# Optimization experiments

Hardware: AMD Instinct MI355X
Metric: run time of the kernel (lower is better)

Reference implementation:

```python
import jax, jax.numpy as jnp
import numpy as np

N_HEADS = 16
HEAD_DIM = 64
SEQ_LEN = 2048
BATCH = 1


def alibi_slopes(n_heads):
    start = 2.0 ** (-8.0 / n_heads)
    return jnp.asarray([start * start ** i for i in range(n_heads)], dtype=jnp.float32)


def setup_inputs() -> dict:
    key = jax.random.key(0)
    kq, kk, kv = jax.random.split(key, 3)
    shape = (BATCH, N_HEADS, SEQ_LEN, HEAD_DIM)
    return {
        "q": jax.random.normal(kq, shape, dtype=jnp.float32),
        "k": jax.random.normal(kk, shape, dtype=jnp.float32),
        "v": jax.random.normal(kv, shape, dtype=jnp.float32),
    }


def reference(q, k, v):
    # q,k,v: [B,H,S,D]
    seq_len = q.shape[2]
    head_dim = q.shape[3]
    scale = 1.0 / np.sqrt(head_dim).astype(np.float32)
    # scores: [B,H,S,S]
    scores = jnp.einsum("bhsd,bhtd->bhst", q, k) * scale
    pos = jnp.arange(seq_len)
    # distances[i, j] = j - i  (pos.unsqueeze(0) - pos.unsqueeze(1))
    distances = (pos[None, :] - pos[:, None]).astype(jnp.float32)  # [S,S]
    slopes = alibi_slopes(q.shape[1])  # [H]
    alibi = slopes[:, None, None] * distances[None, :, :]  # [H,S,S]
    scores = scores + alibi[None]
    attn = jax.nn.softmax(scores, axis=-1)
    return jnp.einsum("bhst,bhtd->bhsd", attn, v)
```

## Files before the change

### kernel.cpp

```cpp
#include <hip/hip_runtime.h>
#include <hip/hip_bf16.h>
#include <stdint.h>

#define N_HEADS 16
#define HEAD_DIM 64
#define SEQ_LEN 2048
#define KVBLK 64
#define NT 16
#define NTILE_TOT (SEQ_LEN / 32)

typedef __bf16 bf16x8 __attribute__((ext_vector_type(8)));
typedef __bf16 bf16x4 __attribute__((ext_vector_type(4)));
typedef short  s16x4  __attribute__((ext_vector_type(4)));
typedef float  f32x4  __attribute__((ext_vector_type(4)));
typedef unsigned int u32x4 __attribute__((ext_vector_type(4)));

#if __has_builtin(__builtin_amdgcn_mfma_f32_16x16x16bf16_1k)
#define HAVE_MFMA16 1
#else
#define HAVE_MFMA16 0
#endif

#if __has_builtin(__builtin_amdgcn_global_load_lds)
#define HAVE_GLL 1
#define GLL16(gsrc, ldst)                                                     \
    __builtin_amdgcn_global_load_lds(                                         \
        (const __attribute__((address_space(1))) void*)(gsrc),                \
        (__attribute__((address_space(3))) void*)(ldst), 16, 0, 0)
#else
#define HAVE_GLL 0
#endif

static __device__ __forceinline__ unsigned pkbf(float a, float b) {
    union { __bf16 h[2]; unsigned u; } t;
    t.h[0] = (__bf16)a; t.h[1] = (__bf16)b;
    return t.u;
}

static __device__ __forceinline__ int vpos(int k) {
#if HAVE_MFMA16
    return ((k & 12) << 2) + ((k & 16) >> 1) + ((k & 3) << 1);
#else
    return k * 2;
#endif
}

__global__ __launch_bounds__(256)
void prep_kernel(const float* __restrict__ k,
                 const float* __restrict__ v,
                 char* __restrict__ kimg,
                 char* __restrict__ vtimg) {
    const int ts  = blockIdx.x;
    const int h   = blockIdx.y;
    const int tid = threadIdx.x;
    const int s0  = ts * 32;
    const size_t blk = ((size_t)h * NTILE_TOT + ts) * 4096;

    const int krow = tid >> 3;
    const int kcol = (tid & 7) * 8;
    const float* ks = k + ((size_t)h * SEQ_LEN + s0 + krow) * HEAD_DIM + kcol;
    f32x4 a = *(const f32x4*)ks;
    f32x4 b = *(const f32x4*)(ks + 4);
    bf16x8 kb;
    #pragma unroll
    for (int i = 0; i < 4; ++i) { kb[i] = (__bf16)a[i]; kb[4 + i] = (__bf16)b[i]; }
    *(bf16x8*)(kimg + blk + krow * 128 + ((kcol * 2) ^ ((krow & 7) << 4))) = kb;

    const int vc = tid & 63;
    const int vr = (tid >> 6) * 8;
    const float* vs = v + ((size_t)h * SEQ_LEN + s0 + vr) * HEAD_DIM + vc;
    bf16x4 vb0, vb1;
    #pragma unroll
    for (int j = 0; j < 4; ++j) {
        vb0[j] = (__bf16)vs[(size_t)j * HEAD_DIM];
        vb1[j] = (__bf16)vs[(size_t)(4 + j) * HEAD_DIM];
    }
    const int swzV = (vc & 7) << 4;
    *(bf16x4*)(vtimg + blk + ((vc * 64 + vpos(vr))     ^ swzV)) = vb0;
    *(bf16x4*)(vtimg + blk + ((vc * 64 + vpos(vr + 4)) ^ swzV)) = vb1;
}

template <bool IMG>
__global__ __launch_bounds__(512, 2)
void attn_alibi_kernel(const float* __restrict__ q,
                       const float* __restrict__ k,
                       const float* __restrict__ v,
                       float* __restrict__ out,
                       const char* __restrict__ kimg,
                       const char* __restrict__ vtimg) {
    const int tid  = threadIdx.x;
    const int wave = tid >> 6;
    const int lane = tid & 63;
    const int col  = lane & 15;
    const int g    = lane >> 4;
    const int half = wave >> 2;
    const int w4   = wave & 3;

    const int h      = blockIdx.y;
    const int qbase  = blockIdx.x * 64 + w4 * 16;
    const int kstart = half * (NT * KVBLK);

    const float* qh = q + (size_t)h * SEQ_LEN * HEAD_DIM;
    const float* kh = k + (size_t)h * SEQ_LEN * HEAD_DIM;
    const float* vh = v + (size_t)h * SEQ_LEN * HEAD_DIM;

    __shared__ alignas(16) char smem[65536];
    char* kbase  = smem + half * 16384;
    char* vtbase = smem + 32768 + half * 16384;

    const float LOG2E  = 1.4426950408889634f;
    const float scale2 = 0.125f * LOG2E;
    const float slope  = exp2f(-0.5f * (float)(h + 1));
    const float slope2 = slope * LOG2E;

    bf16x8 qf[2];
    {
        const float* qr = qh + (size_t)(qbase + col) * HEAD_DIM + g * 8;
        #pragma unroll
        for (int c = 0; c < 2; ++c)
            #pragma unroll
            for (int b = 0; b < 8; ++b) qf[c][b] = (__bf16)qr[c * 32 + b];
    }

    float cb[4][4];
    #pragma unroll
    for (int i = 0; i < 4; ++i)
        #pragma unroll
        for (int r = 0; r < 4; ++r)
            cb[i][r] = slope2 * (float)(i * 16 + g * 4 + r - (qbase + col));

    float m = -1e30f, l = 0.0f;
    f32x4 acc[4];
    #pragma unroll
    for (int dt = 0; dt < 4; ++dt) acc[dt] = (f32x4)0.0f;

    const int hid  = tid & 255;
    const int krow = hid >> 3;
    const int kcol = (hid & 7) * 8;
    const int vc   = hid & 63;
    const int vr   = (hid >> 6) * 8;

    const char* kis = nullptr; const char* vis = nullptr;
    const float* ksrc = nullptr; const float* vsrc = nullptr;
    char* kdst = nullptr; char* vtdst0 = nullptr; char* vtdst1 = nullptr;
    if constexpr (IMG) {
        const size_t base = ((size_t)h * NTILE_TOT + half * (NTILE_TOT / 2)) * 4096
                          + hid * 16;
        kis = kimg + base;  vis = vtimg + base;
#if HAVE_GLL
        kdst   = kbase + w4 * 1024;
        vtdst0 = vtbase + w4 * 1024;
#else
        kdst   = kbase + hid * 16;
        vtdst0 = vtbase + hid * 16;
#endif
    } else {
        ksrc  = kh + (size_t)(kstart + krow) * HEAD_DIM + kcol;
        kdst  = kbase + krow * 128 + ((kcol * 2) ^ ((krow & 7) << 4));
        vsrc  = vh + (size_t)(kstart + vr) * HEAD_DIM + vc;
        const int swzV = (vc & 7) << 4;
        vtdst0 = vtbase + ((vc * 64 + vpos(vr))     ^ swzV);
        vtdst1 = vtbase + ((vc * 64 + vpos(vr + 4)) ^ swzV);
    }

    f32x4 kreg[2], vreg[2];
    f32x4 kr[2][2];
    float vv[2][8];

    if constexpr (IMG) {
#if HAVE_GLL
        #pragma unroll
        for (int sb = 0; sb < 2; ++sb) {
            GLL16(kis + sb * 4096, kdst   + sb * 4096);
            GLL16(vis + sb * 4096, vtdst0 + sb * 4096);
        }
#else
        #pragma unroll
        for (int sb = 0; sb < 2; ++sb) {
            kreg[sb] = *(const f32x4*)(kis + sb * 4096);
            vreg[sb] = *(const f32x4*)(vis + sb * 4096);
            *(f32x4*)(kdst   + sb * 4096) = kreg[sb];
            *(f32x4*)(vtdst0 + sb * 4096) = vreg[sb];
        }
#endif
    } else {
        #pragma unroll
        for (int sb = 0; sb < 2; ++sb) {
            const float* ks = ksrc + (size_t)(sb * 32) * HEAD_DIM;
            const float* vs = vsrc + (size_t)(sb * 32) * HEAD_DIM;
            kr[sb][0] = *(const f32x4*)(ks);
            kr[sb][1] = *(const f32x4*)(ks + 4);
            #pragma unroll
            for (int j = 0; j < 8; ++j) vv[sb][j] = vs[(size_t)j * HEAD_DIM];
            bf16x8 kb16;
            bf16x4 vb0, vb1;
            #pragma unroll
            for (int b = 0; b < 4; ++b) {
                kb16[b] = (__bf16)kr[sb][0][b]; kb16[4 + b] = (__bf16)kr[sb][1][b];
                vb0[b] = (__bf16)vv[sb][b];     vb1[b] = (__bf16)vv[sb][4 + b];
            }
            *(bf16x8*)(kdst   + sb * 4096) = kb16;
            *(bf16x4*)(vtdst0 + sb * 4096) = vb0;
            *(bf16x4*)(vtdst1 + sb * 4096) = vb1;
        }
    }
    __syncthreads();

    for (int t = 0; t < NT; ++t) {
        const int kb  = kstart + t * KVBLK;
        const int buf = t & 1;
        const char* kbuf  = kbase + buf * 8192;
        const char* vtbuf = vtbase + buf * 8192;

#if HAVE_GLL
        if (IMG && t + 1 < NT) {
            const int nb = (t + 1) & 1;
            #pragma unroll
            for (int sb = 0; sb < 2; ++sb) {
                GLL16(kis + (size_t)((t + 1) * 2 + sb) * 4096,
                      kdst + nb * 8192 + sb * 4096);
                GLL16(vis + (size_t)((t + 1) * 2 + sb) * 4096,
                      vtdst0 + nb * 8192 + sb * 4096);
            }
        }
#endif

        f32x4 sacc[4];
        #pragma unroll
        for (int i = 0; i < 4; ++i) sacc[i] = (f32x4)0.0f;
        __builtin_amdgcn_s_setprio(1);
        #pragma unroll
        for (int sb = 0; sb < 2; ++sb) {
            #pragma unroll
            for (int jt = 0; jt < 2; ++jt) {
                const int row = jt * 16 + col;
                const int i   = sb * 2 + jt;
                #pragma unroll
                for (int c = 0; c < 2; ++c) {
                    bf16x8 kf = *(const bf16x8*)(kbuf + sb * 4096 + row * 128
                                                 + ((c * 64 + g * 16) ^ ((row & 7) << 4)));
                    sacc[i] = __builtin_amdgcn_mfma_f32_16x16x32_bf16(kf, qf[c], sacc[i], 0, 0, 0);
                }
            }
        }
        __builtin_amdgcn_s_setprio(0);

        if (t + 1 < NT) {
            if constexpr (IMG) {
#if !HAVE_GLL
                #pragma unroll
                for (int sb = 0; sb < 2; ++sb) {
                    kreg[sb] = *(const f32x4*)(kis + (size_t)((t + 1) * 2 + sb) * 4096);
                    vreg[sb] = *(const f32x4*)(vis + (size_t)((t + 1) * 2 + sb) * 4096);
                }
#endif
            } else {
                #pragma unroll
                for (int sb = 0; sb < 2; ++sb) {
                    const float* ks = ksrc + (size_t)((t + 1) * 64 + sb * 32) * HEAD_DIM;
                    const float* vs = vsrc + (size_t)((t + 1) * 64 + sb * 32) * HEAD_DIM;
                    kr[sb][0] = *(const f32x4*)(ks);
                    kr[sb][1] = *(const f32x4*)(ks + 4);
                    #pragma unroll
                    for (int j = 0; j < 8; ++j) vv[sb][j] = vs[(size_t)j * HEAD_DIM];
                }
            }
        }

        const float skb = slope2 * (float)kb;
        float s[4][4];
        #pragma unroll
        for (int i = 0; i < 4; ++i)
            #pragma unroll
            for (int r = 0; r < 4; ++r)
                s[i][r] = sacc[i][r] * scale2 + (cb[i][r] + skb);

        float x01a = fmaxf(s[0][0], s[0][1]), x01b = fmaxf(s[0][2], s[0][3]);
        float x23a = fmaxf(s[1][0], s[1][1]), x23b = fmaxf(s[1][2], s[1][3]);
        float x45a = fmaxf(s[2][0], s[2][1]), x45b = fmaxf(s[2][2], s[2][3]);
        float x67a = fmaxf(s[3][0], s[3][1]), x67b = fmaxf(s[3][2], s[3][3]);
        float x = fmaxf(fmaxf(fmaxf(x01a, x01b), fmaxf(x23a, x23b)),
                        fmaxf(fmaxf(x45a, x45b), fmaxf(x67a, x67b)));
        x = fmaxf(x, __shfl_xor(x, 16));
        x = fmaxf(x, __shfl_xor(x, 32));

        if (__any(x - m > 8.0f)) {
            float mn    = fmaxf(m, x);
            float alpha = __builtin_amdgcn_exp2f(m - mn);
            m = mn;
            l *= alpha;
            #pragma unroll
            for (int dt = 0; dt < 4; ++dt) acc[dt] *= alpha;
        }

        float p[4][4], y = 0.0f;
        #pragma unroll
        for (int i = 0; i < 4; ++i)
            #pragma unroll
            for (int r = 0; r < 4; ++r) {
                p[i][r] = __builtin_amdgcn_exp2f(s[i][r] - m);
                y += p[i][r];
            }
        l += y;

#if HAVE_MFMA16
        s16x4 pb[4];
        #pragma unroll
        for (int i = 0; i < 4; ++i) {
            bf16x4 pf;
            #pragma unroll
            for (int b = 0; b < 4; ++b) pf[b] = (__bf16)p[i][b];
            pb[i] = __builtin_bit_cast(s16x4, pf);
        }
        __builtin_amdgcn_s_setprio(1);
        #pragma unroll
        for (int dt = 0; dt < 4; ++dt) {
            const int vrow = dt * 16 + col;
            const int off  = (vrow * 64 + g * 16) ^ ((vrow & 7) << 4);
            #pragma unroll
            for (int sb = 0; sb < 2; ++sb) {
                bf16x8 vf = *(const bf16x8*)(vtbuf + sb * 4096 + off);
                bf16x4 vlo = __builtin_shufflevector(vf, vf, 0, 1, 2, 3);
                bf16x4 vhi = __builtin_shufflevector(vf, vf, 4, 5, 6, 7);
                acc[dt] = __builtin_amdgcn_mfma_f32_16x16x16bf16_1k(
                    __builtin_bit_cast(s16x4, vlo), pb[sb * 2 + 0], acc[dt], 0, 0, 0);
                acc[dt] = __builtin_amdgcn_mfma_f32_16x16x16bf16_1k(
                    __builtin_bit_cast(s16x4, vhi), pb[sb * 2 + 1], acc[dt], 0, 0, 0);
            }
        }
        __builtin_amdgcn_s_setprio(0);
#else
        #pragma unroll
        for (int sb = 0; sb < 2; ++sb) {
            unsigned pk00 = pkbf(p[sb * 2][0],     p[sb * 2][1]);
            unsigned pk01 = pkbf(p[sb * 2][2],     p[sb * 2][3]);
            unsigned pk10 = pkbf(p[sb * 2 + 1][0], p[sb * 2 + 1][1]);
            unsigned pk11 = pkbf(p[sb * 2 + 1][2], p[sb * 2 + 1][3]);
            const int srcA = col + ((g & 1) << 5);
            const int srcB = srcA + 16;
            unsigned a00 = __shfl(pk00, srcA), a01 = __shfl(pk01, srcA);
            unsigned a10 = __shfl(pk10, srcA), a11 = __shfl(pk11, srcA);
            unsigned b00 = __shfl(pk00, srcB), b01 = __shfl(pk01, srcB);
            unsigned b10 = __shfl(pk10, srcB), b11 = __shfl(pk11, srcB);
            const bool hi = g >= 2;
            u32x4 pu;
            pu[0] = hi ? a10 : a00;
            pu[1] = hi ? a11 : a01;
            pu[2] = hi ? b10 : b00;
            pu[3] = hi ? b11 : b01;
            bf16x8 pf = __builtin_bit_cast(bf16x8, pu);
            #pragma unroll
            for (int dt = 0; dt < 4; ++dt) {
                const int vrow = dt * 16 + col;
                bf16x8 vf = *(const bf16x8*)(vtbuf + sb * 4096
                                + ((vrow * 64 + g * 16) ^ ((vrow & 7) << 4)));
                acc[dt] = __builtin_amdgcn_mfma_f32_16x16x32_bf16(vf, pf, acc[dt], 0, 0, 0);
            }
        }
#endif

        if (t + 1 < NT) {
            const int nb = (t + 1) & 1;
            if constexpr (IMG) {
#if !HAVE_GLL
                #pragma unroll
                for (int sb = 0; sb < 2; ++sb) {
                    *(f32x4*)(kdst   + nb * 8192 + sb * 4096) = kreg[sb];
                    *(f32x4*)(vtdst0 + nb * 8192 + sb * 4096) = vreg[sb];
                }
#endif
            } else {
                #pragma unroll
                for (int sb = 0; sb < 2; ++sb) {
                    bf16x8 kb16;
                    bf16x4 vb0, vb1;
                    #pragma unroll
                    for (int b = 0; b < 4; ++b) {
                        kb16[b] = (__bf16)kr[sb][0][b]; kb16[4 + b] = (__bf16)kr[sb][1][b];
                        vb0[b] = (__bf16)vv[sb][b];     vb1[b] = (__bf16)vv[sb][4 + b];
                    }
                    *(bf16x8*)(kdst   + nb * 8192 + sb * 4096) = kb16;
                    *(bf16x4*)(vtdst0 + nb * 8192 + sb * 4096) = vb0;
                    *(bf16x4*)(vtdst1 + nb * 8192 + sb * 4096) = vb1;
                }
            }
        }
        __syncthreads();
    }

    l += __shfl_xor(l, 16);
    l += __shfl_xor(l, 32);

    float* eacc = (float*)smem;
    float* eml  = (float*)(smem + 16384);

    if (half == 1) {
        #pragma unroll
        for (int dt = 0; dt < 4; ++dt)
            *(f32x4*)(eacc + w4 * 1024 + col * 64 + dt * 16 + g * 4) = acc[dt];
        if (g == 0) {
            eml[(w4 * 16 + col) * 2 + 0] = m;
            eml[(w4 * 16 + col) * 2 + 1] = l;
        }
    }
    __syncthreads();
    if (half == 0) {
        float m2 = eml[(w4 * 16 + col) * 2 + 0];
        float l2 = eml[(w4 * 16 + col) * 2 + 1];
        float mm = fmaxf(m, m2);
        float a1 = __builtin_amdgcn_exp2f(m - mm);
        float a2 = __builtin_amdgcn_exp2f(m2 - mm);
        float inv = 1.0f / (l * a1 + l2 * a2);
        float* orow = out + ((size_t)h * SEQ_LEN + qbase + col) * HEAD_DIM;
        #pragma unroll
        for (int dt = 0; dt < 4; ++dt) {
            f32x4 o2 = *(const f32x4*)(eacc + w4 * 1024 + col * 64 + dt * 16 + g * 4);
            *(f32x4*)(orow + dt * 16 + g * 4) = (acc[dt] * a1 + o2 * a2) * inv;
        }
    }
}

extern "C" void kernel_launch(void* const* d_in, const int* in_sizes, int n_in,
                              void* d_out, int out_size, void* d_ws, size_t ws_size,
                              hipStream_t stream) {
    const float* q = (const float*)d_in[0];
    const float* k = (const float*)d_in[1];
    const float* v = (const float*)d_in[2];
    float* out = (float*)d_out;

    const size_t imgBytes = (size_t)N_HEADS * NTILE_TOT * 4096;

    dim3 grid(SEQ_LEN / 64, N_HEADS, 1);
    if (ws_size >= 2 * imgBytes) {
        char* kimg  = (char*)d_ws;
        char* vtimg = kimg + imgBytes;
        prep_kernel<<<dim3(NTILE_TOT, N_HEADS, 1), dim3(256, 1, 1), 0, stream>>>(
            k, v, kimg, vtimg);
        attn_alibi_kernel<true><<<grid, dim3(512, 1, 1), 0, stream>>>(
            q, k, v, out, kimg, vtimg);
    } else {
        attn_alibi_kernel<false><<<grid, dim3(512, 1, 1), 0, stream>>>(
            q, k, v, out, nullptr, nullptr);
    }
}
```

Baseline: 47.98 us.

## Replace online softmax max tracking with a precomputed Cauchy-Schwarz score bound

The prep kernel now also computes the maximum squared key norm per head, reduced with shuffles and an atomicMax into a zeroed workspace slot. The attention kernel fixes the softmax offset per query row up front, as the largest ALiBi term in its key half plus scale·|q|·max|k|·1.05. That removes the per-tile max reduction, the cross-lane shuffles and the conditional rescale of the accumulators. In exchange it adds a memset and atomics before attention. The bound can sit well above the true maximum, so probabilities may lose precision or underflow for inputs with large norms. The non-image fallback assumes a key norm of 16.

```diff
diff --git a/kernel.cpp b/kernel.cpp
--- a/kernel.cpp
+++ b/kernel.cpp
@@ -1,6 +1,7 @@
 #include <hip/hip_runtime.h>
 #include <hip/hip_bf16.h>
 #include <stdint.h>
+#include <math.h>
 
 #define N_HEADS 16
 #define HEAD_DIM 64
@@ -49,7 +50,8 @@
 void prep_kernel(const float* __restrict__ k,
                  const float* __restrict__ v,
                  char* __restrict__ kimg,
-                 char* __restrict__ vtimg) {
+                 char* __restrict__ vtimg,
+                 float* __restrict__ knorm) {
     const int ts  = blockIdx.x;
     const int h   = blockIdx.y;
     const int tid = threadIdx.x;
@@ -62,9 +64,19 @@
     f32x4 a = *(const f32x4*)ks;
     f32x4 b = *(const f32x4*)(ks + 4);
     bf16x8 kb;
+    float pn = 0.0f;
     #pragma unroll
-    for (int i = 0; i < 4; ++i) { kb[i] = (__bf16)a[i]; kb[4 + i] = (__bf16)b[i]; }
+    for (int i = 0; i < 4; ++i) {
+        kb[i] = (__bf16)a[i]; kb[4 + i] = (__bf16)b[i];
+        pn += a[i] * a[i] + b[i] * b[i];
+    }
     *(bf16x8*)(kimg + blk + krow * 128 + ((kcol * 2) ^ ((krow & 7) << 4))) = kb;
+
+    pn += __shfl_xor(pn, 1);
+    pn += __shfl_xor(pn, 2);
+    pn += __shfl_xor(pn, 4);
+    if ((tid & 7) == 0)
+        atomicMax((int*)(knorm + h), __float_as_int(pn));
 
     const int vc = tid & 63;
     const int vr = (tid >> 6) * 8;
@@ -87,7 +99,8 @@
                        const float* __restrict__ v,
                        float* __restrict__ out,
                        const char* __restrict__ kimg,
-                       const char* __restrict__ vtimg) {
+                       const char* __restrict__ vtimg,
+                       const float* __restrict__ knorm) {
     const int tid  = threadIdx.x;
     const int wave = tid >> 6;
     const int lane = tid & 63;
@@ -114,22 +127,36 @@
     const float slope2 = slope * LOG2E;
 
     bf16x8 qf[2];
+    float qn2 = 0.0f;
     {
         const float* qr = qh + (size_t)(qbase + col) * HEAD_DIM + g * 8;
         #pragma unroll
         for (int c = 0; c < 2; ++c)
             #pragma unroll
-            for (int b = 0; b < 8; ++b) qf[c][b] = (__bf16)qr[c * 32 + b];
-    }
-
-    float cb[4][4];
+            for (int b = 0; b < 8; ++b) {
+                float x = qr[c * 32 + b];
+                qn2 += x * x;
+                qf[c][b] = (__bf16)x;
+            }
+    }
+    qn2 += __shfl_xor(qn2, 16);
+    qn2 += __shfl_xor(qn2, 32);
+
+    float knmax;
+    if constexpr (IMG) knmax = sqrtf(knorm[h]);
+    else               knmax = 16.0f;
+    const int   kend = kstart + NT * KVBLK;
+    const float m = slope2 * (float)(kend - 1 - (qbase + col))
+                  + scale2 * sqrtf(qn2) * knmax * 1.05f;
+
+    float cbm[4][4];
     #pragma unroll
     for (int i = 0; i < 4; ++i)
         #pragma unroll
         for (int r = 0; r < 4; ++r)
-            cb[i][r] = slope2 * (float)(i * 16 + g * 4 + r - (qbase + col));
-
-    float m = -1e30f, l = 0.0f;
+            cbm[i][r] = slope2 * (float)(i * 16 + g * 4 + r - (qbase + col)) - m;
+
+    float l = 0.0f;
     f32x4 acc[4];
     #pragma unroll
     for (int dt = 0; dt < 4; ++dt) acc[dt] = (f32x4)0.0f;
@@ -268,37 +295,13 @@
         }
 
         const float skb = slope2 * (float)kb;
-        float s[4][4];
+        float p[4][4], y = 0.0f;
         #pragma unroll
         for (int i = 0; i < 4; ++i)
             #pragma unroll
-            for (int r = 0; r < 4; ++r)
-                s[i][r] = sacc[i][r] * scale2 + (cb[i][r] + skb);
-
-        float x01a = fmaxf(s[0][0], s[0][1]), x01b = fmaxf(s[0][2], s[0][3]);
-        float x23a = fmaxf(s[1][0], s[1][1]), x23b = fmaxf(s[1][2], s[1][3]);
-        float x45a = fmaxf(s[2][0], s[2][1]), x45b = fmaxf(s[2][2], s[2][3]);
-        float x67a = fmaxf(s[3][0], s[3][1]), x67b = fmaxf(s[3][2], s[3][3]);
-        float x = fmaxf(fmaxf(fmaxf(x01a, x01b), fmaxf(x23a, x23b)),
-                        fmaxf(fmaxf(x45a, x45b), fmaxf(x67a, x67b)));
-        x = fmaxf(x, __shfl_xor(x, 16));
-        x = fmaxf(x, __shfl_xor(x, 32));
-
-        if (__any(x - m > 8.0f)) {
-            float mn    = fmaxf(m, x);
-            float alpha = __builtin_amdgcn_exp2f(m - mn);
-            m = mn;
-            l *= alpha;
-            #pragma unroll
-            for (int dt = 0; dt < 4; ++dt) acc[dt] *= alpha;
-        }
-
-        float p[4][4], y = 0.0f;
-        #pragma unroll
-        for (int i = 0; i < 4; ++i)
-            #pragma unroll
             for (int r = 0; r < 4; ++r) {
-                p[i][r] = __builtin_amdgcn_exp2f(s[i][r] - m);
+                float sv = sacc[i][r] * scale2 + (cbm[i][r] + skb);
+                p[i][r] = __builtin_amdgcn_exp2f(sv);
                 y += p[i][r];
             }
         l += y;
@@ -429,17 +432,20 @@
     float* out = (float*)d_out;
 
     const size_t imgBytes = (size_t)N_HEADS * NTILE_TOT * 4096;
+    const size_t need = 2 * imgBytes + N_HEADS * sizeof(float);
 
     dim3 grid(SEQ_LEN / 64, N_HEADS, 1);
-    if (ws_size >= 2 * imgBytes) {
-        char* kimg  = (char*)d_ws;
-        char* vtimg = kimg + imgBytes;
+    if (ws_size >= need) {
+        char* kimg   = (char*)d_ws;
+        char* vtimg  = kimg + imgBytes;
+        float* knorm = (float*)(vtimg + imgBytes);
+        hipMemsetAsync(knorm, 0, N_HEADS * sizeof(float), stream);
         prep_kernel<<<dim3(NTILE_TOT, N_HEADS, 1), dim3(256, 1, 1), 0, stream>>>(
-            k, v, kimg, vtimg);
+            k, v, kimg, vtimg, knorm);
         attn_alibi_kernel<true><<<grid, dim3(512, 1, 1), 0, stream>>>(
-            q, k, v, out, kimg, vtimg);
+            q, k, v, out, kimg, vtimg, knorm);
     } else {
         attn_alibi_kernel<false><<<grid, dim3(512, 1, 1), 0, stream>>>(
-            q, k, v, out, nullptr, nullptr);
+            q, k, v, out, nullptr, nullptr, nullptr);
     }
 }
```

After: 90.82 us. +89.3%, slower.
